# Performance work log

Hardware: AMD Instinct MI355X
Metric: run time of the kernel (lower is better)

## Reference

```python
import jax, jax.numpy as jnp
import numpy as np

B, N = 2048, 8192
CART_PIXEL_WIDTH = 640
CART_RESOLUTION = 0.2592


def convert_to_radar_frame(pixel_coords):
    # pixel_coords: [B, N, 2]; metric = R @ pix + t with R = [[0,-res],[res,0]]
    if CART_PIXEL_WIDTH % 2 == 0:
        cart_min_range = (CART_PIXEL_WIDTH / 2 - 0.5) * CART_RESOLUTION
    else:
        cart_min_range = (CART_PIXEL_WIDTH // 2) * CART_RESOLUTION
    x = pixel_coords[..., 0]
    y = pixel_coords[..., 1]
    mx = -CART_RESOLUTION * y + cart_min_range
    my = CART_RESOLUTION * x - cart_min_range
    return jnp.stack([mx, my], axis=-1)


def setup_inputs() -> dict:
    key = jax.random.key(0)
    k1, k2, k3 = jax.random.split(key, 3)
    src = jax.random.uniform(k1, (B, N, 2), dtype=jnp.float32) * CART_PIXEL_WIDTH
    tgt = jax.random.uniform(k2, (B, N, 2), dtype=jnp.float32) * CART_PIXEL_WIDTH
    w = jax.random.uniform(k3, (B, 1, N), dtype=jnp.float32)
    return {"src_coords": src, "tgt_coords": tgt, "weights": w, "convert_from_pixels": 1}


def reference(src_coords, tgt_coords, weights, convert_from_pixels):
    if convert_from_pixels:
        src_coords = convert_to_radar_frame(src_coords)
        tgt_coords = convert_to_radar_frame(tgt_coords)
    # pad 2D -> 3D with zero z, then [B, 3, N]
    src = jnp.pad(src_coords, ((0, 0), (0, 0), (0, 1))).transpose(0, 2, 1)
    tgt = jnp.pad(tgt_coords, ((0, 0), (0, 0), (0, 1))).transpose(0, 2, 1)
    w = jnp.sum(weights, axis=2, keepdims=True) + 0.0001           # [B,1,1]
    src_centroid = jnp.sum(src * weights, axis=2, keepdims=True) / w  # [B,3,1]
    tgt_centroid = jnp.sum(tgt * weights, axis=2, keepdims=True) / w
    src_centered = src - src_centroid
    tgt_centered = tgt - tgt_centroid
    # weighted covariance: [B,3,3]
    W = jnp.einsum('bdn,ben->bde', tgt_centered * weights, src_centered) / w
    U, _, Vh = jnp.linalg.svd(W)
    det_UV = jnp.linalg.det(U) * jnp.linalg.det(Vh)  # det(V) == det(Vh)
    s = jnp.stack([jnp.ones_like(det_UV), jnp.ones_like(det_UV), det_UV], axis=-1)
    # R = U @ diag(1,1,det) @ V^T
    R_tgt_src = jnp.einsum('bij,bj,bjk->bik', U, s, Vh)
    t_tgt_src_insrc = src_centroid - jnp.einsum('bji,bjk->bik', R_tgt_src, tgt_centroid)
    t_src_tgt_intgt = -jnp.einsum('bij,bjk->bik', R_tgt_src, t_tgt_src_insrc)
    return R_tgt_src.transpose(0, 2, 1), t_src_tgt_intgt
```

## Files before the change

### kernel.cpp

```cpp
#include <hip/hip_runtime.h>

#define BATCH 2048
#define NPTS  8192

#define RES 0.2592f
#define CMR 82.8144f

__device__ __forceinline__ float wave_reduce_add(float v) {
    #pragma unroll
    for (int off = 32; off > 0; off >>= 1) v += __shfl_down(v, off, 64);
    return v;
}

__global__ __launch_bounds__(256, 4) void svd_align_kernel(
    const float* __restrict__ src, const float* __restrict__ tgt,
    const float* __restrict__ wts, const int* __restrict__ cvt_flag,
    float* __restrict__ out)
{
    const int b   = blockIdx.x;
    const int tid = threadIdx.x;
    const int convert = *cvt_flag;

    const float4* s4  = (const float4*)(src + (size_t)b * NPTS * 2);
    const float4* t4  = (const float4*)(tgt + (size_t)b * NPTS * 2);
    const float2* w2p = (const float2*)(wts + (size_t)b * NPTS);

    float aW = 0.f, aSx = 0.f, aSy = 0.f, aTx = 0.f, aTy = 0.f;
    float aXX = 0.f, aXY = 0.f, aYX = 0.f, aYY = 0.f;

    #pragma unroll 4
    for (int i = 0; i < 16; ++i) {
        const int k = i * 256 + tid;
        float4 s = s4[k];
        float4 t = t4[k];
        float2 w = w2p[k];

        float sx0, sy0, sx1, sy1, tx0, ty0, tx1, ty1;
        if (convert) {
            sx0 = fmaf(-RES, s.y, CMR);  sy0 = fmaf(RES, s.x, -CMR);
            sx1 = fmaf(-RES, s.w, CMR);  sy1 = fmaf(RES, s.z, -CMR);
            tx0 = fmaf(-RES, t.y, CMR);  ty0 = fmaf(RES, t.x, -CMR);
            tx1 = fmaf(-RES, t.w, CMR);  ty1 = fmaf(RES, t.z, -CMR);
        } else {
            sx0 = s.x; sy0 = s.y; sx1 = s.z; sy1 = s.w;
            tx0 = t.x; ty0 = t.y; tx1 = t.z; ty1 = t.w;
        }

        {
            float wv = w.x;
            float wtx = wv * tx0, wty = wv * ty0;
            aW  += wv;
            aSx = fmaf(wv, sx0, aSx);  aSy = fmaf(wv, sy0, aSy);
            aTx += wtx;                aTy += wty;
            aXX = fmaf(wtx, sx0, aXX); aXY = fmaf(wtx, sy0, aXY);
            aYX = fmaf(wty, sx0, aYX); aYY = fmaf(wty, sy0, aYY);
        }
        {
            float wv = w.y;
            float wtx = wv * tx1, wty = wv * ty1;
            aW  += wv;
            aSx = fmaf(wv, sx1, aSx);  aSy = fmaf(wv, sy1, aSy);
            aTx += wtx;                aTy += wty;
            aXX = fmaf(wtx, sx1, aXX); aXY = fmaf(wtx, sy1, aXY);
            aYX = fmaf(wty, sx1, aYX); aYY = fmaf(wty, sy1, aYY);
        }
    }

    aW  = wave_reduce_add(aW);
    aSx = wave_reduce_add(aSx);  aSy = wave_reduce_add(aSy);
    aTx = wave_reduce_add(aTx);  aTy = wave_reduce_add(aTy);
    aXX = wave_reduce_add(aXX);  aXY = wave_reduce_add(aXY);
    aYX = wave_reduce_add(aYX);  aYY = wave_reduce_add(aYY);

    __shared__ float red[4][9];
    const int wave = tid >> 6;
    if ((tid & 63) == 0) {
        red[wave][0] = aW;
        red[wave][1] = aSx; red[wave][2] = aSy;
        red[wave][3] = aTx; red[wave][4] = aTy;
        red[wave][5] = aXX; red[wave][6] = aXY;
        red[wave][7] = aYX; red[wave][8] = aYY;
    }
    __syncthreads();

    if (tid == 0) {
        double Sw = 0, Ssx = 0, Ssy = 0, Stx = 0, Sty = 0;
        double Sxx = 0, Sxy = 0, Syx = 0, Syy = 0;
        #pragma unroll
        for (int i = 0; i < 4; ++i) {
            Sw  += red[i][0];
            Ssx += red[i][1]; Ssy += red[i][2];
            Stx += red[i][3]; Sty += red[i][4];
            Sxx += red[i][5]; Sxy += red[i][6];
            Syx += red[i][7]; Syy += red[i][8];
        }

        const double wd  = Sw + 1e-4;
        const double scx = Ssx / wd, scy = Ssy / wd;
        const double tcx = Stx / wd, tcy = Sty / wd;

        const double W00 = (Sxx - tcx * Ssx - scx * Stx + tcx * scx * Sw) / wd;
        const double W01 = (Sxy - tcx * Ssy - scy * Stx + tcx * scy * Sw) / wd;
        const double W10 = (Syx - tcy * Ssx - scx * Sty + tcy * scx * Sw) / wd;
        const double W11 = (Syy - tcy * Ssy - scy * Sty + tcy * scy * Sw) / wd;

        const double det = W00 * W11 - W01 * W10;

        double R00, R01, R10, R11, dsign;
        if (det >= 0.0) {
            const double p = W00 + W11;
            const double q = W10 - W01;
            double r = sqrt(p * p + q * q);
            if (r > 0.0) {
                R00 = p / r;  R01 = -q / r;
                R10 = q / r;  R11 = p / r;
            } else {
                R00 = 1.0; R01 = 0.0; R10 = 0.0; R11 = 1.0;
            }
            dsign = 1.0;
        } else {
            const double p = W00 - W11;
            const double q = W01 + W10;
            const double r = sqrt(p * p + q * q);
            R00 = p / r;   R01 = q / r;
            R10 = q / r;   R11 = -p / r;
            dsign = -1.0;
        }

        const double tt0 = scx - (R00 * tcx + R10 * tcy);
        const double tt1 = scy - (R01 * tcx + R11 * tcy);
        const double o0 = -(R00 * tt0 + R01 * tt1);
        const double o1 = -(R10 * tt0 + R11 * tt1);

        float* oR = out + (size_t)b * 9;
        oR[0] = (float)R00; oR[1] = (float)R10; oR[2] = 0.f;
        oR[3] = (float)R01; oR[4] = (float)R11; oR[5] = 0.f;
        oR[6] = 0.f;        oR[7] = 0.f;        oR[8] = (float)dsign;

        float* oT = out + (size_t)BATCH * 9 + (size_t)b * 3;
        oT[0] = (float)o0; oT[1] = (float)o1; oT[2] = 0.f;
    }
}

extern "C" void kernel_launch(void* const* d_in, const int* in_sizes, int n_in,
                              void* d_out, int out_size, void* d_ws, size_t ws_size,
                              hipStream_t stream) {
    const float* src = (const float*)d_in[0];
    const float* tgt = (const float*)d_in[1];
    const float* wts = (const float*)d_in[2];
    const int*   cvt = (const int*)d_in[3];
    float* out = (float*)d_out;

    svd_align_kernel<<<BATCH, 256, 0, stream>>>(src, tgt, wts, cvt, out);
}
```

Before: 60.05 us.

## Stream inputs through triple-buffered LDS with async global_load_lds and hoist pixel conversion

Each wave now copies its slice of src, tgt and weights straight into LDS with global_load_lds, keeping three chunks in flight. Explicit vmcnt waits pace the pipeline, and the register accumulation then reads from LDS. The per-point pixel-to-metric conversion is dropped from the inner loop and applied once to the reduced sums as an affine transform in double precision. This aims to hide memory latency and remove per-point ALU work, at the cost of more LDS use, hand-written waitcnt logic and a different summation path that could change floating-point rounding.

```diff
diff --git a/kernel.cpp b/kernel.cpp
--- a/kernel.cpp
+++ b/kernel.cpp
@@ -3,8 +3,9 @@
 #define BATCH 2048
 #define NPTS  8192
 
-#define RES 0.2592f
-#define CMR 82.8144f
+#define BUF_F   640
+#define WAVE_F  (3 * BUF_F)
+#define LDS_F   (4 * WAVE_F)
 
 __device__ __forceinline__ float wave_reduce_add(float v) {
     #pragma unroll
@@ -12,57 +13,82 @@
     return v;
 }
 
-__global__ __launch_bounds__(256, 4) void svd_align_kernel(
+__device__ __forceinline__ void gld16(const float* g, float* l) {
+    __builtin_amdgcn_global_load_lds(
+        (const __attribute__((address_space(1))) void*)g,
+        (__attribute__((address_space(3))) void*)l, 16, 0, 0);
+}
+__device__ __forceinline__ void gld4(const float* g, float* l) {
+    __builtin_amdgcn_global_load_lds(
+        (const __attribute__((address_space(1))) void*)g,
+        (__attribute__((address_space(3))) void*)l, 4, 0, 0);
+}
+
+__global__ __launch_bounds__(256) void svd_align_kernel(
     const float* __restrict__ src, const float* __restrict__ tgt,
     const float* __restrict__ wts, const int* __restrict__ cvt_flag,
     float* __restrict__ out)
 {
     const int b   = blockIdx.x;
     const int tid = threadIdx.x;
-    const int convert = *cvt_flag;
+    const int wv  = tid >> 6;
+    const int ln  = tid & 63;
 
-    const float4* s4  = (const float4*)(src + (size_t)b * NPTS * 2);
-    const float4* t4  = (const float4*)(tgt + (size_t)b * NPTS * 2);
-    const float2* w2p = (const float2*)(wts + (size_t)b * NPTS);
+    __shared__ __align__(16) float lds[LDS_F];
+    __shared__ float red[4][9];
+
+    const float* srcW = src + (size_t)b * (NPTS * 2) + wv * 4096;
+    const float* tgtW = tgt + (size_t)b * (NPTS * 2) + wv * 4096;
+    const float* wtsW = wts + (size_t)b * NPTS + wv * 2048;
+    float* myLds = &lds[wv * WAVE_F];
+
+    auto ISSUE = [&](int c) {
+        float* sb = myLds + (c % 3) * BUF_F;
+        gld16(srcW + c * 256 + ln * 4, sb);
+        gld16(tgtW + c * 256 + ln * 4, sb + 256);
+        gld4 (wtsW + c * 128 + ln,      sb + 512);
+        gld4 (wtsW + c * 128 + 64 + ln, sb + 576);
+    };
+
+    ISSUE(0); ISSUE(1); ISSUE(2);
 
     float aW = 0.f, aSx = 0.f, aSy = 0.f, aTx = 0.f, aTy = 0.f;
     float aXX = 0.f, aXY = 0.f, aYX = 0.f, aYY = 0.f;
 
-    #pragma unroll 4
-    for (int i = 0; i < 16; ++i) {
-        const int k = i * 256 + tid;
-        float4 s = s4[k];
-        float4 t = t4[k];
-        float2 w = w2p[k];
+    #pragma unroll
+    for (int c = 0; c < 16; ++c) {
+        if (c <= 13)      asm volatile("s_waitcnt vmcnt(8)" ::: "memory");
+        else if (c == 14) asm volatile("s_waitcnt vmcnt(4)" ::: "memory");
+        else              asm volatile("s_waitcnt vmcnt(0)" ::: "memory");
+        __builtin_amdgcn_sched_barrier(0);
 
-        float sx0, sy0, sx1, sy1, tx0, ty0, tx1, ty1;
-        if (convert) {
-            sx0 = fmaf(-RES, s.y, CMR);  sy0 = fmaf(RES, s.x, -CMR);
-            sx1 = fmaf(-RES, s.w, CMR);  sy1 = fmaf(RES, s.z, -CMR);
-            tx0 = fmaf(-RES, t.y, CMR);  ty0 = fmaf(RES, t.x, -CMR);
-            tx1 = fmaf(-RES, t.w, CMR);  ty1 = fmaf(RES, t.z, -CMR);
-        } else {
-            sx0 = s.x; sy0 = s.y; sx1 = s.z; sy1 = s.w;
-            tx0 = t.x; ty0 = t.y; tx1 = t.z; ty1 = t.w;
-        }
+        const float* sb = myLds + (c % 3) * BUF_F;
+        const float4 s  = *(const float4*)(sb + (ln << 2));
+        const float4 t  = *(const float4*)(sb + 256 + (ln << 2));
+        const float2 w2 = *(const float2*)(sb + 512 + (ln << 1));
+
+        asm volatile("s_waitcnt lgkmcnt(0)" ::: "memory");
+        __builtin_amdgcn_sched_barrier(0);
+
+        if (c + 3 < 16) ISSUE(c + 3);
 
         {
-            float wv = w.x;
-            float wtx = wv * tx0, wty = wv * ty0;
-            aW  += wv;
-            aSx = fmaf(wv, sx0, aSx);  aSy = fmaf(wv, sy0, aSy);
-            aTx += wtx;                aTy += wty;
-            aXX = fmaf(wtx, sx0, aXX); aXY = fmaf(wtx, sy0, aXY);
-            aYX = fmaf(wty, sx0, aYX); aYY = fmaf(wty, sy0, aYY);
+            const float wgt = w2.x;
+            const float wtx = wgt * t.x, wty = wgt * t.y;
+            aW  += wgt;
+            aSx = fmaf(wgt, s.x, aSx);  aSy = fmaf(wgt, s.y, aSy);
+            aTx += wtx;                 aTy += wty;
+            aXX = fmaf(wtx, s.x, aXX);  aXY = fmaf(wtx, s.y, aXY);
+            aYX = fmaf(wty, s.x, aYX);  aYY = fmaf(wty, s.y, aYY);
         }
         {
-            float wv = w.y;
-            float wtx = wv * tx1, wty = wv * ty1;
-            aW  += wv;
-            aSx = fmaf(wv, sx1, aSx);  aSy = fmaf(wv, sy1, aSy);
-            aTx += wtx;                aTy += wty;
-            aXX = fmaf(wtx, sx1, aXX); aXY = fmaf(wtx, sy1, aXY);
-            aYX = fmaf(wty, sx1, aYX); aYY = fmaf(wty, sy1, aYY);
+            const float wgt = w2.y;
+            const float wtx = wgt * t.z, wty = wgt * t.w;
+            aW  += wgt;
+            aSx = fmaf(wgt, s.z, aSx);  aSy = fmaf(wgt, s.w, aSy);
+            aTx += wtx;                 aTy += wty;
+            aXX = fmaf(wtx, s.z, aXX);  aXY = fmaf(wtx, s.w, aXY);
+            aYX = fmaf(wty, s.z, aYX);  aYY = fmaf(wty, s.w, aYY);
         }
     }
 
@@ -72,14 +98,12 @@
     aXX = wave_reduce_add(aXX);  aXY = wave_reduce_add(aXY);
     aYX = wave_reduce_add(aYX);  aYY = wave_reduce_add(aYY);
 
-    __shared__ float red[4][9];
-    const int wave = tid >> 6;
-    if ((tid & 63) == 0) {
-        red[wave][0] = aW;
-        red[wave][1] = aSx; red[wave][2] = aSy;
-        red[wave][3] = aTx; red[wave][4] = aTy;
-        red[wave][5] = aXX; red[wave][6] = aXY;
-        red[wave][7] = aYX; red[wave][8] = aYY;
+    if (ln == 0) {
+        red[wv][0] = aW;
+        red[wv][1] = aSx; red[wv][2] = aSy;
+        red[wv][3] = aTx; red[wv][4] = aTy;
+        red[wv][5] = aXX; red[wv][6] = aXY;
+        red[wv][7] = aYX; red[wv][8] = aYY;
     }
     __syncthreads();
 
@@ -93,6 +117,21 @@
             Stx += red[i][3]; Sty += red[i][4];
             Sxx += red[i][5]; Sxy += red[i][6];
             Syx += red[i][7]; Syy += red[i][8];
+        }
+
+        if (*cvt_flag) {
+            const double r  = 0.2592;
+            const double cc = (640.0 / 2 - 0.5) * 0.2592;
+            const double nSsx = -r * Ssy + cc * Sw;
+            const double nSsy =  r * Ssx - cc * Sw;
+            const double nStx = -r * Sty + cc * Sw;
+            const double nSty =  r * Stx - cc * Sw;
+            const double nSxx =  r * r * Syy - r * cc * (Sty + Ssy) + cc * cc * Sw;
+            const double nSxy = -r * r * Syx + r * cc * (Sty + Ssx) - cc * cc * Sw;
+            const double nSyx = -r * r * Sxy + r * cc * (Stx + Ssy) - cc * cc * Sw;
+            const double nSyy =  r * r * Sxx - r * cc * (Stx + Ssx) + cc * cc * Sw;
+            Ssx = nSsx; Ssy = nSsy; Stx = nStx; Sty = nSty;
+            Sxx = nSxx; Sxy = nSxy; Syx = nSyx; Syy = nSyy;
         }
 
         const double wd  = Sw + 1e-4;
@@ -110,10 +149,10 @@
         if (det >= 0.0) {
             const double p = W00 + W11;
             const double q = W10 - W01;
-            double r = sqrt(p * p + q * q);
-            if (r > 0.0) {
-                R00 = p / r;  R01 = -q / r;
-                R10 = q / r;  R11 = p / r;
+            double r2 = sqrt(p * p + q * q);
+            if (r2 > 0.0) {
+                R00 = p / r2;  R01 = -q / r2;
+                R10 = q / r2;  R11 = p / r2;
             } else {
                 R00 = 1.0; R01 = 0.0; R10 = 0.0; R11 = 1.0;
             }
@@ -121,9 +160,9 @@
         } else {
             const double p = W00 - W11;
             const double q = W01 + W10;
-            const double r = sqrt(p * p + q * q);
-            R00 = p / r;   R01 = q / r;
-            R10 = q / r;   R11 = -p / r;
+            const double r2 = sqrt(p * p + q * q);
+            R00 = p / r2;   R01 = q / r2;
+            R10 = q / r2;   R11 = -p / r2;
             dsign = -1.0;
         }
 
```

New measurement: 65.91 us. 9.8% more time.

## Apply pixel-to-metric conversion algebraically to reduced sums; widen weight loads

Applied to the files above, without the earlier changes.

Moves the affine pixel-to-radar conversion out of the per-point loop. It is applied once to the accumulated moment sums in double precision, using the linearity of the sums. Each thread now handles 4 consecutive points per iteration, with a float4 weight load and two float4 loads each for src and tgt. This removes per-point FMAs and the branch on the flag. The risk is reduced float accuracy, because raw pixel values around 640 give larger second moments, which are accumulated in fp32 before conversion.

```diff
diff --git a/kernel.cpp b/kernel.cpp
--- a/kernel.cpp
+++ b/kernel.cpp
@@ -2,9 +2,6 @@
 
 #define BATCH 2048
 #define NPTS  8192
-
-#define RES 0.2592f
-#define CMR 82.8144f
 
 __device__ __forceinline__ float wave_reduce_add(float v) {
     #pragma unroll
@@ -19,52 +16,38 @@
 {
     const int b   = blockIdx.x;
     const int tid = threadIdx.x;
-    const int convert = *cvt_flag;
 
-    const float4* s4  = (const float4*)(src + (size_t)b * NPTS * 2);
-    const float4* t4  = (const float4*)(tgt + (size_t)b * NPTS * 2);
-    const float2* w2p = (const float2*)(wts + (size_t)b * NPTS);
+    const float4* s4 = (const float4*)(src + (size_t)b * NPTS * 2);
+    const float4* t4 = (const float4*)(tgt + (size_t)b * NPTS * 2);
+    const float4* w4 = (const float4*)(wts + (size_t)b * NPTS);
 
     float aW = 0.f, aSx = 0.f, aSy = 0.f, aTx = 0.f, aTy = 0.f;
     float aXX = 0.f, aXY = 0.f, aYX = 0.f, aYY = 0.f;
 
-    #pragma unroll 4
-    for (int i = 0; i < 16; ++i) {
-        const int k = i * 256 + tid;
-        float4 s = s4[k];
-        float4 t = t4[k];
-        float2 w = w2p[k];
+#define ACCPT(wgt, sx, sy, tx, ty) do {                                \
+        const float wtx = (wgt) * (tx), wty = (wgt) * (ty);            \
+        aW  += (wgt);                                                  \
+        aSx = fmaf((wgt), (sx), aSx);  aSy = fmaf((wgt), (sy), aSy);   \
+        aTx += wtx;                    aTy += wty;                     \
+        aXX = fmaf(wtx, (sx), aXX);    aXY = fmaf(wtx, (sy), aXY);     \
+        aYX = fmaf(wty, (sx), aYX);    aYY = fmaf(wty, (sy), aYY);     \
+    } while (0)
 
-        float sx0, sy0, sx1, sy1, tx0, ty0, tx1, ty1;
-        if (convert) {
-            sx0 = fmaf(-RES, s.y, CMR);  sy0 = fmaf(RES, s.x, -CMR);
-            sx1 = fmaf(-RES, s.w, CMR);  sy1 = fmaf(RES, s.z, -CMR);
-            tx0 = fmaf(-RES, t.y, CMR);  ty0 = fmaf(RES, t.x, -CMR);
-            tx1 = fmaf(-RES, t.w, CMR);  ty1 = fmaf(RES, t.z, -CMR);
-        } else {
-            sx0 = s.x; sy0 = s.y; sx1 = s.z; sy1 = s.w;
-            tx0 = t.x; ty0 = t.y; tx1 = t.z; ty1 = t.w;
-        }
+    #pragma unroll 2
+    for (int i = 0; i < 8; ++i) {
+        const int q = i * 512 + (tid << 1);
+        const float4 sA = s4[q];
+        const float4 sB = s4[q + 1];
+        const float4 tA = t4[q];
+        const float4 tB = t4[q + 1];
+        const float4 w  = w4[i * 256 + tid];
 
-        {
-            float wv = w.x;
-            float wtx = wv * tx0, wty = wv * ty0;
-            aW  += wv;
-            aSx = fmaf(wv, sx0, aSx);  aSy = fmaf(wv, sy0, aSy);
-            aTx += wtx;                aTy += wty;
-            aXX = fmaf(wtx, sx0, aXX); aXY = fmaf(wtx, sy0, aXY);
-            aYX = fmaf(wty, sx0, aYX); aYY = fmaf(wty, sy0, aYY);
-        }
-        {
-            float wv = w.y;
-            float wtx = wv * tx1, wty = wv * ty1;
-            aW  += wv;
-            aSx = fmaf(wv, sx1, aSx);  aSy = fmaf(wv, sy1, aSy);
-            aTx += wtx;                aTy += wty;
-            aXX = fmaf(wtx, sx1, aXX); aXY = fmaf(wtx, sy1, aXY);
-            aYX = fmaf(wty, sx1, aYX); aYY = fmaf(wty, sy1, aYY);
-        }
+        ACCPT(w.x, sA.x, sA.y, tA.x, tA.y);
+        ACCPT(w.y, sA.z, sA.w, tA.z, tA.w);
+        ACCPT(w.z, sB.x, sB.y, tB.x, tB.y);
+        ACCPT(w.w, sB.z, sB.w, tB.z, tB.w);
     }
+#undef ACCPT
 
     aW  = wave_reduce_add(aW);
     aSx = wave_reduce_add(aSx);  aSy = wave_reduce_add(aSy);
@@ -95,6 +78,21 @@
             Syx += red[i][7]; Syy += red[i][8];
         }
 
+        if (*cvt_flag) {
+            const double r  = 0.2592;
+            const double cc = (640.0 / 2 - 0.5) * 0.2592;
+            const double nSsx = -r * Ssy + cc * Sw;
+            const double nSsy =  r * Ssx - cc * Sw;
+            const double nStx = -r * Sty + cc * Sw;
+            const double nSty =  r * Stx - cc * Sw;
+            const double nSxx =  r * r * Syy - r * cc * (Sty + Ssy) + cc * cc * Sw;
+            const double nSxy = -r * r * Syx + r * cc * (Sty + Ssx) - cc * cc * Sw;
+            const double nSyx = -r * r * Sxy + r * cc * (Stx + Ssy) - cc * cc * Sw;
+            const double nSyy =  r * r * Sxx - r * cc * (Stx + Ssx) + cc * cc * Sw;
+            Ssx = nSsx; Ssy = nSsy; Stx = nStx; Sty = nSty;
+            Sxx = nSxx; Sxy = nSxy; Syx = nSyx; Syy = nSyy;
+        }
+
         const double wd  = Sw + 1e-4;
         const double scx = Ssx / wd, scy = Ssy / wd;
         const double tcx = Stx / wd, tcy = Sty / wd;
@@ -110,10 +108,10 @@
         if (det >= 0.0) {
             const double p = W00 + W11;
             const double q = W10 - W01;
-            double r = sqrt(p * p + q * q);
-            if (r > 0.0) {
-                R00 = p / r;  R01 = -q / r;
-                R10 = q / r;  R11 = p / r;
+            double r2 = sqrt(p * p + q * q);
+            if (r2 > 0.0) {
+                R00 = p / r2;  R01 = -q / r2;
+                R10 = q / r2;  R11 = p / r2;
             } else {
                 R00 = 1.0; R01 = 0.0; R10 = 0.0; R11 = 1.0;
             }
@@ -121,9 +119,9 @@
         } else {
             const double p = W00 - W11;
             const double q = W01 + W10;
-            const double r = sqrt(p * p + q * q);
-            R00 = p / r;   R01 = q / r;
-            R10 = q / r;   R11 = -p / r;
+            const double r2 = sqrt(p * p + q * q);
+            R00 = p / r2;   R01 = q / r2;
+            R10 = q / r2;   R11 = -p / r2;
             dsign = -1.0;
         }
 
```

Measured after the change: 58.71 us. -2.2%, faster.
